# Kernel optimization log

Measured on AMD Instinct MI355X. Metric: run time of the kernel, lower is better.

Reference implementation:

```python
import jax, jax.numpy as jnp
import numpy as np

N_MIN = 16
N_TABLES = 16
PER_LEVEL_SCALE = 1.3195079565048218
MAX_TABLE = 2 ** 19
H1, H2, H3 = 1, 2654435761, 805459861
OFFS = np.array([[0,0,0],[0,0,1],[0,1,0],[0,1,1],[1,0,0],[1,0,1],[1,1,0],[1,1,1]], dtype=np.int32)

def _levels():
    N_l, sizes, max_direct = [], [], 0
    for i in range(N_TABLES):
        res = int(np.ceil(N_MIN * np.exp(i * np.log(PER_LEVEL_SCALE)) - 1.0)) + 1
        ts = res ** 3
        ts = ts if ts % 8 == 0 else ((ts + 7) // 8) * 8
        ts = min(MAX_TABLE, ts)
        if ts == res ** 3:
            max_direct = i
        N_l.append(res); sizes.append(ts)
    return N_l, sizes, max_direct

N_L, SIZES, MAX_DIRECT = _levels()

def hash_encode(pos, grids):
    # pos: [N,3] in [0,1); grids: [16, MAX_TABLE, 2] (levels padded to MAX_TABLE)
    feats = []
    for l in range(N_TABLES):
        uvz = pos * jnp.float32(N_L[l])
        iuv_f = jnp.floor(uvz)
        f = uvz - iuv_f                                   # fractional part [N,3]
        corners = iuv_f.astype(jnp.int32)[:, None, :] + OFFS[None]  # [N,8,3]
        if l <= MAX_DIRECT:
            R = N_L[l]
            idx = (corners[..., 2] * (R * R) + corners[..., 1] * R + corners[..., 0]) % SIZES[l]
        else:
            cu = corners.astype(jnp.uint32)
            h = (cu[..., 0] * jnp.uint32(H1)) ^ (cu[..., 1] * jnp.uint32(H2)) ^ (cu[..., 2] * jnp.uint32(H3))
            idx = (h % jnp.uint32(SIZES[l])).astype(jnp.int32)
        c = grids[l][idx]                                 # gather -> [N,8,2]
        fx, fy, fz = f[:, 0:1], f[:, 1:2], f[:, 2:3]
        c00 = c[:, 0] * (1 - fx) + c[:, 4] * fx
        c01 = c[:, 1] * (1 - fx) + c[:, 5] * fx
        c10 = c[:, 2] * (1 - fx) + c[:, 6] * fx
        c11 = c[:, 3] * (1 - fx) + c[:, 7] * fx
        c0 = c00 * (1 - fy) + c10 * fy
        c1 = c01 * (1 - fy) + c11 * fy
        feats.append(c0 * (1 - fz) + c1 * fy)  # NOTE: c1*fy (not fz) replicates source exactly
    return jnp.concatenate(feats, axis=-1)  # [N, 32]

def setup_inputs():
    key = jax.random.key(0)
    ks = jax.random.split(key, 7)
    N = 1048576  # max_samples(512) * batch_size(2048)
    x = jax.random.uniform(ks[0], (N, 19), dtype=jnp.float32)  # pos(3) in [0,1) + dir feats(16)
    grids = (jax.random.uniform(ks[1], (N_TABLES, MAX_TABLE, 2), dtype=jnp.float32) * 2.0 - 1.0) * 1e-4
    h = 64
    w_sigma1 = jax.random.normal(ks[2], (32, h), dtype=jnp.float32) / np.sqrt(32).astype(np.float32)
    w_sigma2 = jax.random.normal(ks[3], (h, 16), dtype=jnp.float32) / np.sqrt(h).astype(np.float32)
    w_c1 = jax.random.normal(ks[4], (32, h), dtype=jnp.float32) / np.sqrt(32).astype(np.float32)
    w_c2 = jax.random.normal(ks[5], (h, h), dtype=jnp.float32) / np.sqrt(h).astype(np.float32)
    w_c3 = jax.random.normal(ks[6], (h, 3), dtype=jnp.float32) / np.sqrt(h).astype(np.float32)
    return {"x": x, "grids": grids, "w_sigma1": w_sigma1, "w_sigma2": w_sigma2,
            "w_c1": w_c1, "w_c2": w_c2, "w_c3": w_c3}

def reference(x, grids, w_sigma1, w_sigma2, w_c1, w_c2, w_c3):
    pos, direc = x[:, :3], x[:, 3:]
    enc = hash_encode(pos, grids)                       # [N,32]
    out = jax.nn.relu(enc @ w_sigma1) @ w_sigma2        # [N,16]
    sigma = out[:, 0]
    ci = jnp.concatenate([direc, out], axis=-1)         # [N,32]
    color = jax.nn.sigmoid(jax.nn.relu(jax.nn.relu(ci @ w_c1) @ w_c2) @ w_c3)  # [N,3]
    return jnp.concatenate([color, sigma[:, None]], axis=-1)  # [N,4]
```

## Files before the change

### kernel.cpp

```cpp
#include <hip/hip_runtime.h>
#include <math.h>


#define BLOCK 256
#define NTAB  (16*524288)
#define PITCH 88

constexpr int      kNL[16] = {16,22,28,37,49,65,85,112,148,195,257,338,446,589,777,1025};
constexpr unsigned kSZ[16] = {4096u,10648u,21952u,50656u,117656u,274632u,
                              524288u,524288u,524288u,524288u,524288u,
                              524288u,524288u,524288u,524288u,524288u};

typedef __attribute__((ext_vector_type(8))) short short8;
typedef __attribute__((ext_vector_type(4))) float float4v;

__device__ __forceinline__ short f2bf(float f) {
    unsigned u = __float_as_uint(f);
    unsigned r = u + 0x7fffu + ((u >> 16) & 1u);
    return (short)(r >> 16);
}
__device__ __forceinline__ float bf2f(short h) {
    return __uint_as_float(((unsigned)(unsigned short)h) << 16);
}
__device__ __forceinline__ unsigned pk2(float a, float b) {
    return ((unsigned)(unsigned short)f2bf(b) << 16) | (unsigned)(unsigned short)f2bf(a);
}
__device__ __forceinline__ float pe0(unsigned u) { return __uint_as_float(u << 16); }
__device__ __forceinline__ float pe1(unsigned u) { return __uint_as_float(u & 0xffff0000u); }

__device__ __forceinline__ unsigned trilerp_pack(const unsigned* vv, float fx, float fy, float fz)
{
    const float w0x = 1.f-fx, w0y = 1.f-fy, w0z = 1.f-fz;
    float e0, e1;
    {
        float c00 = pe0(vv[0])*w0x + pe0(vv[4])*fx;
        float c01 = pe0(vv[1])*w0x + pe0(vv[5])*fx;
        float c10 = pe0(vv[2])*w0x + pe0(vv[6])*fx;
        float c11 = pe0(vv[3])*w0x + pe0(vv[7])*fx;
        float c0 = c00*w0y + c10*fy;
        float c1 = c01*w0y + c11*fy;
        e0 = c0*w0z + c1*fy;
    }
    {
        float c00 = pe1(vv[0])*w0x + pe1(vv[4])*fx;
        float c01 = pe1(vv[1])*w0x + pe1(vv[5])*fx;
        float c10 = pe1(vv[2])*w0x + pe1(vv[6])*fx;
        float c11 = pe1(vv[3])*w0x + pe1(vv[7])*fx;
        float c0 = c00*w0y + c10*fy;
        float c1 = c01*w0y + c11*fy;
        e1 = c0*w0z + c1*fy;
    }
    return pk2(e0, e1);
}

__global__ __launch_bounds__(BLOCK)
void prep_all(const float* __restrict__ x, const float* __restrict__ grids,
              const float* __restrict__ w1, const float* __restrict__ w2,
              const float* __restrict__ wc1, const float* __restrict__ wc2,
              const float* __restrict__ wc3,
              float4* __restrict__ pos4, unsigned* __restrict__ tbu,
              uint4* __restrict__ wf, int n, int nTabBlk, int nPosBlk)
{
    const int b = blockIdx.x;
    if (b < nTabBlk) {
        int i = b * BLOCK + threadIdx.x;
        if (i < NTAB) {
            float2 v = ((const float2*)grids)[i];
            tbu[i] = pk2(v.x, v.y);
        }
    } else if (b < nTabBlk + nPosBlk) {
        int i = (b - nTabBlk) * BLOCK + threadIdx.x;
        if (i < n) {
            const float* xr = x + (size_t)i * 19;
            pos4[i] = make_float4(xr[0], xr[1], xr[2], 0.f);
        }
    } else {
        int lane = threadIdx.x;
        if (lane < 64) {
            int cn = lane & 15, q = lane >> 4;
            auto pack8 = [](const float* src, int stride) -> uint4 {
                uint4 r;
                r.x = pk2(src[0*stride], src[1*stride]);
                r.y = pk2(src[2*stride], src[3*stride]);
                r.z = pk2(src[4*stride], src[5*stride]);
                r.w = pk2(src[6*stride], src[7*stride]);
                return r;
            };
            int f = 0;
            for (int nt = 0; nt < 4; ++nt)
                wf[(f++)*64 + lane] = pack8(w1 + (q*8)*64 + nt*16 + cn, 64);
            for (int c = 0; c < 2; ++c)
                wf[(f++)*64 + lane] = pack8(w2 + (c*32 + q*8)*16 + cn, 16);
            for (int nt = 0; nt < 4; ++nt)
                wf[(f++)*64 + lane] = pack8(wc1 + (q*8)*64 + nt*16 + cn, 64);
            for (int c = 0; c < 2; ++c)
                for (int nt = 0; nt < 4; ++nt)
                    wf[(f++)*64 + lane] = pack8(wc2 + (c*32 + q*8)*64 + nt*16 + cn, 64);
            for (int c = 0; c < 2; ++c) {
                if (cn < 3) wf[(f++)*64 + lane] = pack8(wc3 + (c*32 + q*8)*3 + cn, 3);
                else { uint4 z; z.x = z.y = z.z = z.w = 0u; wf[(f++)*64 + lane] = z; }
            }
        }
    }
}

template<int L>
__device__ __forceinline__ void gather4(const float4* __restrict__ pos4,
                                        const unsigned* __restrict__ tball,
                                        unsigned* __restrict__ encu,
                                        int n, int p0, int cnt)
{
    constexpr unsigned S = kSZ[L];
    constexpr unsigned H2c = 2654435761u, H3c = 805459861u;
    constexpr int R = kNL[L];
    (void)R;
    const unsigned* __restrict__ tbu = tball + (size_t)L * 524288u;

    unsigned vv[4][8];
    float fxa[4], fya[4], fza[4];
    #pragma unroll
    for (int q = 0; q < 4; ++q) {
        if (q >= cnt) continue;
        float4 p = pos4[p0+q];
        const float Rf = (float)kNL[L];
        float ux = p.x*Rf, uy = p.y*Rf, uz = p.z*Rf;
        float gx = floorf(ux), gy = floorf(uy), gz = floorf(uz);
        fxa[q] = ux-gx; fya[q] = uy-gy; fza[q] = uz-gz;
        int ix = (int)gx, iy = (int)gy, iz = (int)gz;

        unsigned tc[4];
        #pragma unroll
        for (int c = 0; c < 4; ++c) {
            int yb = c >> 1, zb = c & 1;
            tc[c] = (unsigned)(iy+yb)*H2c ^ (unsigned)(iz+zb)*H3c;
        }
        if ((ix & 1) == 0) {
            #pragma unroll
            for (int c = 0; c < 4; ++c) {
                unsigned idx0 = ((unsigned)ix ^ tc[c]) & (S-1u);
                uint2 pr = *(const uint2*)(tbu + (idx0 & ~1u));
                unsigned swp = idx0 & 1u;
                vv[q][c]   = swp ? pr.y : pr.x;
                vv[q][4+c] = swp ? pr.x : pr.y;
            }
        } else {
            #pragma unroll
            for (int c = 0; c < 4; ++c) {
                unsigned idx0 = ((unsigned)ix     ^ tc[c]) & (S-1u);
                unsigned idx1 = ((unsigned)(ix+1) ^ tc[c]) & (S-1u);
                vv[q][c]   = tbu[idx0];
                vv[q][4+c] = tbu[idx1];
            }
        }
    }

    unsigned pkd[4];
    #pragma unroll
    for (int q = 0; q < 4; ++q) {
        if (q >= cnt) continue;
        pkd[q] = trilerp_pack(vv[q], fxa[q], fya[q], fza[q]);
    }

    unsigned* d = encu + (size_t)L*n + p0;
    if (cnt == 4) {
        uint4 o; o.x = pkd[0]; o.y = pkd[1]; o.z = pkd[2]; o.w = pkd[3];
        *(uint4*)d = o;
    } else {
        for (int q = 0; q < cnt; ++q) d[q] = pkd[q];
    }
}

__global__ __launch_bounds__(BLOCK)
void enc_all(const float4* __restrict__ pos4, const unsigned* __restrict__ tball,
             unsigned* __restrict__ encu, int n, int byA)
{
    const int bx = blockIdx.x;
    const int by = blockIdx.y;

    if (by < byA) {
        int p0 = (by*BLOCK + threadIdx.x) * 4;
        if (p0 >= n) return;
        int cnt = min(4, n - p0);
        switch (bx) {
            case 0: gather4< 6>(pos4,tball,encu,n,p0,cnt); break;
            case 1: gather4< 7>(pos4,tball,encu,n,p0,cnt); break;
            case 2: gather4< 8>(pos4,tball,encu,n,p0,cnt); break;
            case 3: gather4< 9>(pos4,tball,encu,n,p0,cnt); break;
            case 4: gather4<10>(pos4,tball,encu,n,p0,cnt); break;
            case 5: gather4<11>(pos4,tball,encu,n,p0,cnt); break;
            case 6: gather4<12>(pos4,tball,encu,n,p0,cnt); break;
            case 7: gather4<13>(pos4,tball,encu,n,p0,cnt); break;
        }
    } else {
        int q4 = (n + 3) / 4;
        int quarter = bx & 3;
        int jb = quarter * q4;
        int je = min(n, jb + q4);
        int p0 = jb + ((by-byA)*BLOCK + threadIdx.x) * 4;
        if (p0 >= je) return;
        int cnt = min(4, je - p0);
        if (bx < 4) gather4<14>(pos4,tball,encu,n,p0,cnt);
        else        gather4<15>(pos4,tball,encu,n,p0,cnt);
    }
}

template<int LV>
__device__ __forceinline__ void enc_addr(float4 p, const unsigned* __restrict__ tball,
                                         unsigned vv[8], float& fx, float& fy, float& fz)
{
    constexpr int R = kNL[LV];
    constexpr unsigned S = kSZ[LV];
    constexpr unsigned H2c = 2654435761u, H3c = 805459861u;
    const unsigned* __restrict__ tb = tball + (size_t)LV * 524288u;
    const float Rf = (float)R;
    float ux = p.x*Rf, uy = p.y*Rf, uz = p.z*Rf;
    float gx = floorf(ux), gy = floorf(uy), gz = floorf(uz);
    fx = ux-gx; fy = uy-gy; fz = uz-gz;
    int ix = (int)gx, iy = (int)gy, iz = (int)gz;

    if (LV >= 3) {
        unsigned tc[4];
        #pragma unroll
        for (int c = 0; c < 4; ++c) {
            int yb = c >> 1, zb = c & 1;
            tc[c] = (unsigned)(iy+yb)*H2c ^ (unsigned)(iz+zb)*H3c;
        }
        if ((ix & 1) == 0) {
            #pragma unroll
            for (int c = 0; c < 4; ++c) {
                unsigned h0 = (unsigned)ix ^ tc[c];
                unsigned base = (h0 & ~1u) % S;
                uint2 pr = *(const uint2*)(tb + base);
                unsigned swp = h0 & 1u;
                vv[c]   = swp ? pr.y : pr.x;
                vv[4+c] = swp ? pr.x : pr.y;
            }
        } else {
            #pragma unroll
            for (int c = 0; c < 4; ++c) {
                vv[c]   = tb[(((unsigned)ix)     ^ tc[c]) % S];
                vv[4+c] = tb[(((unsigned)(ix+1)) ^ tc[c]) % S];
            }
        }
    } else {
        #pragma unroll
        for (int j = 0; j < 8; ++j) {
            int ox = ix + ((j>>2)&1);
            int oy = iy + ((j>>1)&1);
            int oz = iz + (j&1);
            vv[j] = tb[(unsigned)((oz*(R*R) + oy*R + ox) % (int)S)];
        }
    }
}

__device__ __forceinline__ short8 ldfrag(const uint4* __restrict__ wf, int f, int lane) {
    union { uint4 u; short8 s; } cv;
    cv.u = wf[f*64 + lane];
    return cv.s;
}

__global__ __launch_bounds__(BLOCK)
void mlp_mfma(const float* __restrict__ x,
              const float4* __restrict__ pos4,
              const unsigned* __restrict__ tbu,
              const unsigned* __restrict__ encu,
              const uint4* __restrict__ wf,
              float* __restrict__ out, int n)
{
    __shared__ unsigned short s_scr[4][2][16*PITCH];
    __shared__ float s_sig[4][16];
    __shared__ float s_col[4][16][4];
    __shared__ float s_dir[4][304];
    __shared__ unsigned s_lowB[6][64];

    const int t = threadIdx.x;
    const int lane = t & 63;
    const int wave = t >> 6;
    const int m = lane & 15;
    const int q = lane >> 4;
    const int cn = m;
    const int blk = blockIdx.x * 64;
    const int pt  = blk + wave*16 + m;
    const int ptc = pt < n ? pt : n - 1;
    const int p0w = blk + wave*16;

    const float4v zero = {0.f, 0.f, 0.f, 0.f};

    unsigned encv[4];
    #pragma unroll
    for (int i = 0; i < 4; ++i) {
        int lv = q*4 + i;
        if (lv >= 6) encv[i] = encu[(size_t)lv*n + ptc];
    }

    {
        int npts = n - p0w; if (npts > 16) npts = 16; if (npts < 0) npts = 0;
        int nfl = npts * 19;
        const float* xs = x + (size_t)p0w * 19;
        float* sd = s_dir[wave];
        #pragma unroll
        for (int it = 0; it < 5; ++it) {
            int idx = it*64 + lane;
            if (idx < nfl) sd[idx] = xs[idx];
        }
    }

    {
        int pp = blk + lane; if (pp >= n) pp = n - 1;
        float4 p = pos4[pp];
        unsigned vv[8]; float fx, fy, fz;
        switch (wave) {
            case 0:  enc_addr<0>(p, tbu, vv, fx, fy, fz); break;
            case 1:  enc_addr<1>(p, tbu, vv, fx, fy, fz); break;
            case 2:  enc_addr<2>(p, tbu, vv, fx, fy, fz); break;
            default: enc_addr<3>(p, tbu, vv, fx, fy, fz); break;
        }
        s_lowB[wave][lane] = trilerp_pack(vv, fx, fy, fz);
    }
    if (lane < 32) {
        int lv = 4 + (wave >> 1);
        int pb2 = (wave & 1)*32 + lane;
        int pp = blk + pb2; if (pp >= n) pp = n - 1;
        float4 p = pos4[pp];
        unsigned vv[8]; float fx, fy, fz;
        if (lv == 4) enc_addr<4>(p, tbu, vv, fx, fy, fz);
        else         enc_addr<5>(p, tbu, vv, fx, fy, fz);
        s_lowB[lv][pb2] = trilerp_pack(vv, fx, fy, fz);
    }
    __syncthreads();

    union { unsigned u[4]; short8 s; } a1;
    #pragma unroll
    for (int i = 0; i < 4; ++i) {
        int lv = q*4 + i;
        if (lv < 6) a1.u[i] = s_lowB[lv][wave*16 + m];
        else        a1.u[i] = encv[i];
    }

    short8 bw1[4], bw2[2], bwc1[4];
    #pragma unroll
    for (int nt = 0; nt < 4; ++nt) bw1[nt] = ldfrag(wf, nt, lane);
    #pragma unroll
    for (int c = 0; c < 2; ++c)    bw2[c]  = ldfrag(wf, 4 + c, lane);
    #pragma unroll
    for (int nt = 0; nt < 4; ++nt) bwc1[nt] = ldfrag(wf, 6 + nt, lane);

    float4v h[4];
    #pragma unroll
    for (int nt = 0; nt < 4; ++nt) {
        h[nt] = __builtin_amdgcn_mfma_f32_16x16x32_bf16(a1.s, bw1[nt], zero, 0, 0, 0);
        #pragma unroll
        for (int r = 0; r < 4; ++r) h[nt][r] = fmaxf(h[nt][r], 0.f);
    }

    unsigned short* sA = &s_scr[wave][0][0];
    unsigned short* sB = &s_scr[wave][1][0];
    #pragma unroll
    for (int nt = 0; nt < 4; ++nt)
        #pragma unroll
        for (int r = 0; r < 4; ++r)
            sA[(q*4+r)*PITCH + nt*16 + cn] = (unsigned short)f2bf(h[nt][r]);
    short8 ah[2];
    #pragma unroll
    for (int c = 0; c < 2; ++c)
        ah[c] = *(const short8*)&sA[m*PITCH + c*32 + q*8];

    float4v o = __builtin_amdgcn_mfma_f32_16x16x32_bf16(ah[0], bw2[0], zero, 0, 0, 0);
    o = __builtin_amdgcn_mfma_f32_16x16x32_bf16(ah[1], bw2[1], o, 0, 0, 0);
    if (cn == 0) {
        #pragma unroll
        for (int r = 0; r < 4; ++r) s_sig[wave][q*4+r] = o[r];
    }

    #pragma unroll
    for (int r = 0; r < 4; ++r)
        sB[(q*4+r)*PITCH + cn] = (unsigned short)f2bf(o[r]);
    short8 ov = *(const short8*)&sB[m*PITCH + (q >= 2 ? (q-2)*8 : 0)];

    union { unsigned u[4]; short8 s; } ci_hi, ci_lo;
    if (q < 2) {
        const float* sd = s_dir[wave];
        int rm = ptc - p0w; if (rm < 0) rm = 0;
        #pragma unroll
        for (int i = 0; i < 4; ++i) {
            float d0 = sd[rm*19 + 3 + q*8 + 2*i];
            float d1 = sd[rm*19 + 3 + q*8 + 2*i + 1];
            short h0 = f2bf(d0), h1 = f2bf(d1);
            ci_hi.u[i] = ((unsigned)(unsigned short)h1 << 16) | (unsigned)(unsigned short)h0;
            short l0 = f2bf(d0 - bf2f(h0)), l1 = f2bf(d1 - bf2f(h1));
            ci_lo.u[i] = ((unsigned)(unsigned short)l1 << 16) | (unsigned)(unsigned short)l0;
        }
    } else {
        ci_hi.s = ov;
        #pragma unroll
        for (int i = 0; i < 4; ++i) ci_lo.u[i] = 0u;
    }

    float4v hc[4];
    #pragma unroll
    for (int nt = 0; nt < 4; ++nt) {
        hc[nt] = __builtin_amdgcn_mfma_f32_16x16x32_bf16(ci_hi.s, bwc1[nt], zero, 0, 0, 0);
        hc[nt] = __builtin_amdgcn_mfma_f32_16x16x32_bf16(ci_lo.s, bwc1[nt], hc[nt], 0, 0, 0);
        #pragma unroll
        for (int r = 0; r < 4; ++r) hc[nt][r] = fmaxf(hc[nt][r], 0.f);
    }

    short8 bwc2[2][4], bwc3[2];
    #pragma unroll
    for (int c = 0; c < 2; ++c)
        #pragma unroll
        for (int nt = 0; nt < 4; ++nt)
            bwc2[c][nt] = ldfrag(wf, 10 + c*4 + nt, lane);
    #pragma unroll
    for (int c = 0; c < 2; ++c) bwc3[c] = ldfrag(wf, 18 + c, lane);

    #pragma unroll
    for (int nt = 0; nt < 4; ++nt)
        #pragma unroll
        for (int r = 0; r < 4; ++r) {
            float v = hc[nt][r];
            short hi = f2bf(v);
            sA[(q*4+r)*PITCH + nt*16 + cn] = (unsigned short)hi;
            sB[(q*4+r)*PITCH + nt*16 + cn] = (unsigned short)f2bf(v - bf2f(hi));
        }
    short8 ghi[2], glo[2];
    #pragma unroll
    for (int c = 0; c < 2; ++c) {
        ghi[c] = *(const short8*)&sA[m*PITCH + c*32 + q*8];
        glo[c] = *(const short8*)&sB[m*PITCH + c*32 + q*8];
    }

    float4v g[4];
    #pragma unroll
    for (int nt = 0; nt < 4; ++nt) {
        float4v acc = __builtin_amdgcn_mfma_f32_16x16x32_bf16(ghi[0], bwc2[0][nt], zero, 0, 0, 0);
        acc = __builtin_amdgcn_mfma_f32_16x16x32_bf16(glo[0], bwc2[0][nt], acc, 0, 0, 0);
        acc = __builtin_amdgcn_mfma_f32_16x16x32_bf16(ghi[1], bwc2[1][nt], acc, 0, 0, 0);
        acc = __builtin_amdgcn_mfma_f32_16x16x32_bf16(glo[1], bwc2[1][nt], acc, 0, 0, 0);
        #pragma unroll
        for (int r = 0; r < 4; ++r) acc[r] = fmaxf(acc[r], 0.f);
        g[nt] = acc;
    }

    #pragma unroll
    for (int nt = 0; nt < 4; ++nt)
        #pragma unroll
        for (int r = 0; r < 4; ++r) {
            float v = g[nt][r];
            short hi = f2bf(v);
            sA[(q*4+r)*PITCH + nt*16 + cn] = (unsigned short)hi;
            sB[(q*4+r)*PITCH + nt*16 + cn] = (unsigned short)f2bf(v - bf2f(hi));
        }
    short8 uhi[2], ulo[2];
    #pragma unroll
    for (int c = 0; c < 2; ++c) {
        uhi[c] = *(const short8*)&sA[m*PITCH + c*32 + q*8];
        ulo[c] = *(const short8*)&sB[m*PITCH + c*32 + q*8];
    }

    float4v col = __builtin_amdgcn_mfma_f32_16x16x32_bf16(uhi[0], bwc3[0], zero, 0, 0, 0);
    col = __builtin_amdgcn_mfma_f32_16x16x32_bf16(ulo[0], bwc3[0], col, 0, 0, 0);
    col = __builtin_amdgcn_mfma_f32_16x16x32_bf16(uhi[1], bwc3[1], col, 0, 0, 0);
    col = __builtin_amdgcn_mfma_f32_16x16x32_bf16(ulo[1], bwc3[1], col, 0, 0, 0);
    #pragma unroll
    for (int r = 0; r < 4; ++r)
        col[r] = 1.f / (1.f + __expf(-col[r]));

    if (cn < 3) {
        #pragma unroll
        for (int r = 0; r < 4; ++r) s_col[wave][q*4+r][cn] = col[r];
    }

    __builtin_amdgcn_s_waitcnt(0);
    int pfi = lane >> 2, c4 = lane & 3;
    int pout = blk + wave*16 + pfi;
    if (pout < n) {
        float v = (c4 == 3) ? s_sig[wave][pfi] : s_col[wave][pfi][c4];
        out[(size_t)pout*4 + c4] = v;
    }
}

extern "C" void kernel_launch(void* const* d_in, const int* in_sizes, int n_in,
                              void* d_out, int out_size, void* d_ws, size_t ws_size,
                              hipStream_t stream) {
    const float* x     = (const float*)d_in[0];
    const float* grids = (const float*)d_in[1];
    const float* w1    = (const float*)d_in[2];
    const float* w2    = (const float*)d_in[3];
    const float* wc1   = (const float*)d_in[4];
    const float* wc2   = (const float*)d_in[5];
    const float* wc3   = (const float*)d_in[6];
    float* out = (float*)d_out;

    int n = in_sizes[0] / 19;
    size_t encB = (size_t)16 * n * sizeof(unsigned);
    size_t posB = (size_t)n * sizeof(float4);
    size_t tabB = (size_t)NTAB * sizeof(unsigned);

    char* p = (char*)d_ws;
    unsigned* encu = (unsigned*)p;
    float4*   pos4 = (float4*)(p + encB);
    unsigned* tbu  = (unsigned*)(p + encB + posB);
    uint4*    wf   = (uint4*)(p + encB + posB + tabB);

    int nTabBlk = (NTAB + BLOCK - 1) / BLOCK;
    int nPosBlk = (n + BLOCK - 1) / BLOCK;
    prep_all<<<nTabBlk + nPosBlk + 1, BLOCK, 0, stream>>>(
        x, grids, w1, w2, wc1, wc2, wc3, pos4, tbu, wf, n, nTabBlk, nPosBlk);

    int byA = (n + BLOCK*4 - 1) / (BLOCK*4);
    int q4  = (n + 3) / 4;
    int byB = (q4 + BLOCK*4 - 1) / (BLOCK*4);
    dim3 ge(8, byA + byB);
    enc_all<<<ge, BLOCK, 0, stream>>>(pos4, tbu, encu, n, byA);

    mlp_mfma<<<(n + 63) / 64, BLOCK, 0, stream>>>(x, pos4, tbu, encu, wf, out, n);
}
```

Baseline: 532.4 us.

## Pipeline hash-grid encoding and MLP across point chunks with mixed kernels

Splits the points into four chunks and launches kernels that combine encoding of chunk c with MLP evaluation of chunk c-1, with rows of blocks interleaved inside one grid. The aim is to overlap the gather-heavy, memory-bound encoding with the MFMA-heavy MLP so that both the memory system and the compute units stay busy, instead of running two serial full-size kernels. The cost is more launches, a block-role branch that may raise register and LDS pressure in the combined kernel (it now holds both bodies), and chunked encoding that may touch the hash tables less uniformly.

```diff
diff --git a/kernel.cpp b/kernel.cpp
--- a/kernel.cpp
+++ b/kernel.cpp
@@ -112,8 +112,6 @@
 {
     constexpr unsigned S = kSZ[L];
     constexpr unsigned H2c = 2654435761u, H3c = 805459861u;
-    constexpr int R = kNL[L];
-    (void)R;
     const unsigned* __restrict__ tbu = tball + (size_t)L * 524288u;
 
     unsigned vv[4][8];
@@ -170,17 +168,16 @@
     }
 }
 
-__global__ __launch_bounds__(BLOCK)
-void enc_all(const float4* __restrict__ pos4, const unsigned* __restrict__ tball,
-             unsigned* __restrict__ encu, int n, int byA)
-{
-    const int bx = blockIdx.x;
-    const int by = blockIdx.y;
-
-    if (by < byA) {
-        int p0 = (by*BLOCK + threadIdx.x) * 4;
-        if (p0 >= n) return;
-        int cnt = min(4, n - p0);
+__device__ __forceinline__ void enc_body(int bx, int row, int base, int len, int byAc,
+                                         const float4* __restrict__ pos4,
+                                         const unsigned* __restrict__ tball,
+                                         unsigned* __restrict__ encu, int n)
+{
+    if (row < byAc) {
+        int p0 = base + (row*BLOCK + (int)threadIdx.x) * 4;
+        int pend = base + len;
+        if (p0 >= pend) return;
+        int cnt = min(4, pend - p0);
         switch (bx) {
             case 0: gather4< 6>(pos4,tball,encu,n,p0,cnt); break;
             case 1: gather4< 7>(pos4,tball,encu,n,p0,cnt); break;
@@ -192,11 +189,11 @@
             case 7: gather4<13>(pos4,tball,encu,n,p0,cnt); break;
         }
     } else {
-        int q4 = (n + 3) / 4;
+        int q4 = (len + 3) / 4;
         int quarter = bx & 3;
-        int jb = quarter * q4;
-        int je = min(n, jb + q4);
-        int p0 = jb + ((by-byA)*BLOCK + threadIdx.x) * 4;
+        int jb = base + quarter * q4;
+        int je = min(base + len, jb + q4);
+        int p0 = jb + ((row-byAc)*BLOCK + (int)threadIdx.x) * 4;
         if (p0 >= je) return;
         int cnt = min(4, je - p0);
         if (bx < 4) gather4<14>(pos4,tball,encu,n,p0,cnt);
@@ -259,13 +256,12 @@
     return cv.s;
 }
 
-__global__ __launch_bounds__(BLOCK)
-void mlp_mfma(const float* __restrict__ x,
-              const float4* __restrict__ pos4,
-              const unsigned* __restrict__ tbu,
-              const unsigned* __restrict__ encu,
-              const uint4* __restrict__ wf,
-              float* __restrict__ out, int n)
+__device__ void mlp_body(const float* __restrict__ x,
+                         const float4* __restrict__ pos4,
+                         const unsigned* __restrict__ tbu,
+                         const unsigned* __restrict__ encu,
+                         const uint4* __restrict__ wf,
+                         float* __restrict__ out, int n, int blk)
 {
     __shared__ unsigned short s_scr[4][2][16*PITCH];
     __shared__ float s_sig[4][16];
@@ -279,7 +275,6 @@
     const int m = lane & 15;
     const int q = lane >> 4;
     const int cn = m;
-    const int blk = blockIdx.x * 64;
     const int pt  = blk + wave*16 + m;
     const int ptc = pt < n ? pt : n - 1;
     const int p0w = blk + wave*16;
@@ -306,7 +301,7 @@
     }
 
     {
-        int pp = blk + lane; if (pp >= n) pp = n - 1;
+        int pp = blk + lane; if (pp >= n) pp = n - 1; if (pp < 0) pp = 0;
         float4 p = pos4[pp];
         unsigned vv[8]; float fx, fy, fz;
         switch (wave) {
@@ -320,7 +315,7 @@
     if (lane < 32) {
         int lv = 4 + (wave >> 1);
         int pb2 = (wave & 1)*32 + lane;
-        int pp = blk + pb2; if (pp >= n) pp = n - 1;
+        int pp = blk + pb2; if (pp >= n) pp = n - 1; if (pp < 0) pp = 0;
         float4 p = pos4[pp];
         unsigned vv[8]; float fx, fy, fz;
         if (lv == 4) enc_addr<4>(p, tbu, vv, fx, fy, fz);
@@ -478,6 +473,44 @@
         float v = (c4 == 3) ? s_sig[wave][pfi] : s_col[wave][pfi][c4];
         out[(size_t)pout*4 + c4] = v;
     }
+}
+
+__global__ __launch_bounds__(BLOCK)
+void enc_chunk(const float4* __restrict__ pos4, const unsigned* __restrict__ tball,
+               unsigned* __restrict__ encu, int n, int base, int len, int byAc)
+{
+    enc_body((int)blockIdx.x, (int)blockIdx.y, base, len, byAc, pos4, tball, encu, n);
+}
+
+__global__ __launch_bounds__(BLOCK)
+void mix_kernel(const float* __restrict__ x, const float4* __restrict__ pos4,
+                const unsigned* __restrict__ tbu, unsigned* __restrict__ encu,
+                const uint4* __restrict__ wf, float* __restrict__ out, int n,
+                int encBase, int encLen, int byAc, int E, int R,
+                int mlpBase, int mlpEnd)
+{
+    const int r = blockIdx.y;
+    const int er  = (int)(((long long)r     * E) / R);
+    const int er1 = (int)(((long long)(r+1) * E) / R);
+    if (er1 > er) {
+        enc_body((int)blockIdx.x, er, encBase, encLen, byAc, pos4, tbu, encu, n);
+    } else {
+        int mrow = r - er;
+        int blk = mlpBase + (mrow*8 + (int)blockIdx.x)*64;
+        if (blk >= mlpEnd) return;
+        mlp_body(x, pos4, tbu, encu, wf, out, n, blk);
+    }
+}
+
+__global__ __launch_bounds__(BLOCK)
+void mlp_chunk(const float* __restrict__ x, const float4* __restrict__ pos4,
+               const unsigned* __restrict__ tbu, const unsigned* __restrict__ encu,
+               const uint4* __restrict__ wf, float* __restrict__ out, int n,
+               int pbase, int pend)
+{
+    int blk = pbase + (int)blockIdx.x*64;
+    if (blk >= pend) return;
+    mlp_body(x, pos4, tbu, encu, wf, out, n, blk);
 }
 
 extern "C" void kernel_launch(void* const* d_in, const int* in_sizes, int n_in,
@@ -508,11 +541,52 @@
     prep_all<<<nTabBlk + nPosBlk + 1, BLOCK, 0, stream>>>(
         x, grids, w1, w2, wc1, wc2, wc3, pos4, tbu, wf, n, nTabBlk, nPosBlk);
 
-    int byA = (n + BLOCK*4 - 1) / (BLOCK*4);
-    int q4  = (n + 3) / 4;
-    int byB = (q4 + BLOCK*4 - 1) / (BLOCK*4);
-    dim3 ge(8, byA + byB);
-    enc_all<<<ge, BLOCK, 0, stream>>>(pos4, tbu, encu, n, byA);
-
-    mlp_mfma<<<(n + 63) / 64, BLOCK, 0, stream>>>(x, pos4, tbu, encu, wf, out, n);
-}
+    const int NCH = 4;
+    int nc = ((n + NCH - 1) / NCH + 1023) & ~1023;
+    int cb[NCH+1];
+    for (int i = 0; i <= NCH; ++i) {
+        long long b = (long long)i * nc;
+        cb[i] = (int)(b < n ? b : n);
+    }
+
+    auto encRows = [&](int len, int& byAc) {
+        byAc = (len + BLOCK*4 - 1) / (BLOCK*4);
+        int q4 = (len + 3) / 4;
+        int byBc = (q4 + BLOCK*4 - 1) / (BLOCK*4);
+        return byAc + byBc;
+    };
+
+    {
+        int len0 = cb[1] - cb[0];
+        if (len0 > 0) {
+            int byA0; int E0 = encRows(len0, byA0);
+            enc_chunk<<<dim3(8, E0), BLOCK, 0, stream>>>(pos4, tbu, encu, n, cb[0], len0, byA0);
+        }
+    }
+    for (int c = 1; c < NCH; ++c) {
+        int lenE = cb[c+1] - cb[c];
+        int lenM = cb[c] - cb[c-1];
+        int Mrows = (lenM + 511) / 512;
+        if (lenE > 0 && lenM > 0) {
+            int byAc; int E = encRows(lenE, byAc);
+            int R = E + Mrows;
+            mix_kernel<<<dim3(8, R), BLOCK, 0, stream>>>(
+                x, pos4, tbu, encu, wf, out, n,
+                cb[c], lenE, byAc, E, R, cb[c-1], cb[c]);
+        } else if (lenM > 0) {
+            mlp_chunk<<<dim3(Mrows*8), BLOCK, 0, stream>>>(
+                x, pos4, tbu, encu, wf, out, n, cb[c-1], cb[c]);
+        } else if (lenE > 0) {
+            int byAc; int E = encRows(lenE, byAc);
+            enc_chunk<<<dim3(8, E), BLOCK, 0, stream>>>(pos4, tbu, encu, n, cb[c], lenE, byAc);
+        }
+    }
+    {
+        int lenT = cb[NCH] - cb[NCH-1];
+        if (lenT > 0) {
+            int Mt = (lenT + 63) / 64;
+            mlp_chunk<<<dim3(Mt), BLOCK, 0, stream>>>(
+                x, pos4, tbu, encu, wf, out, n, cb[NCH-1], cb[NCH]);
+        }
+    }
+}
```

After: 605.3 us. +13.7%, slower.
